# Kernel optimization log

Hardware: AMD Instinct MI355X
Metric: run time of the kernel (lower is better)

The kernel has to match this reference:

```python
import jax, jax.numpy as jnp
import numpy as np

C, H, P = 128, 4, 8  # d_model, n_heads, n_points (n_levels=1)
D = C // H


def setup_inputs() -> dict:
    key = jax.random.key(0)
    ks = jax.random.split(key, 14)
    B, Y, X = 2, 200, 200
    N = Y * X
    s = 0.05
    inp = {
        "query": jax.random.normal(ks[0], (B, N, C), jnp.float32),
        "query_pos": jax.random.normal(ks[1], (B, N, C), jnp.float32),
        # MSDeformAttn params
        "Wv": jax.random.normal(ks[2], (C, C), jnp.float32) * s,
        "bv": jnp.zeros((C,), jnp.float32),
        "Woff": jax.random.normal(ks[3], (C, H * P * 2), jnp.float32) * s,
        "boff": jax.random.normal(ks[4], (H * P * 2,), jnp.float32) * s,
        "Wattn": jax.random.normal(ks[5], (C, H * P), jnp.float32) * s,
        "battn": jnp.zeros((H * P,), jnp.float32),
        "Wout1": jax.random.normal(ks[6], (C, C), jnp.float32) * s,  # MSDeformAttn.output_proj
        "bout1": jnp.zeros((C,), jnp.float32),
        "Wout2": jax.random.normal(ks[7], (C, C), jnp.float32) * s,  # wrapper output_proj
        "bout2": jnp.zeros((C,), jnp.float32),
        "Y": Y,
        "X": X,
    }
    return inp


def _deform_attn(q, v_in, Wv, bv, Woff, boff, Wattn, battn, Wout1, bout1, Y, X):
    B, N, _ = q.shape
    # reference points: grid centers, stacked (y, x) normalized (as in source)
    ref_y = (jnp.arange(Y, dtype=jnp.float32) + 0.5) / Y
    ref_x = (jnp.arange(X, dtype=jnp.float32) + 0.5) / X
    ry, rx = jnp.meshgrid(ref_y, ref_x, indexing="ij")
    ref = jnp.stack([ry.reshape(-1), rx.reshape(-1)], -1)  # (N, 2)

    value = (v_in @ Wv + bv).reshape(B, Y, X, H, D).transpose(0, 3, 1, 2, 4)  # (B,H,Y,X,D)
    off = (q @ Woff + boff).reshape(B, N, H, P, 2)
    attn = jax.nn.softmax((q @ Wattn + battn).reshape(B, N, H, P), axis=-1)

    # offset normalizer = (W, H) = (X, Y); loc = ref + off/norm  (faithful to source)
    norm = jnp.array([X, Y], jnp.float32)
    loc = ref[None, :, None, None, :] + off / norm  # (B,N,H,P,2)

    # grid_sample bilinear, align_corners=False, zero padding; channel 0 = x, 1 = y
    gx = loc[..., 0] * X - 0.5
    gy = loc[..., 1] * Y - 0.5
    x0 = jnp.floor(gx)
    y0 = jnp.floor(gy)
    wx1 = gx - x0
    wy1 = gy - y0
    x0i = x0.astype(jnp.int32)
    y0i = y0.astype(jnp.int32)

    b_idx = jnp.arange(B)[:, None, None, None]
    h_idx = jnp.arange(H)[None, None, :, None]

    def gather(yi, xi, w):
        valid = (yi >= 0) & (yi < Y) & (xi >= 0) & (xi < X)
        yc = jnp.clip(yi, 0, Y - 1)
        xc = jnp.clip(xi, 0, X - 1)
        v = value[b_idx, h_idx, yc, xc]  # (B,N,H,P,D)
        return v * (w * valid)[..., None]

    sampled = (
        gather(y0i, x0i, (1 - wy1) * (1 - wx1))
        + gather(y0i, x0i + 1, (1 - wy1) * wx1)
        + gather(y0i + 1, x0i, wy1 * (1 - wx1))
        + gather(y0i + 1, x0i + 1, wy1 * wx1)
    )
    out = (sampled * attn[..., None]).sum(axis=3).reshape(B, N, C)
    return out @ Wout1 + bout1


def reference(query, query_pos, Wv, bv, Woff, boff, Wattn, battn, Wout1, bout1, Wout2, bout2, Y, X):
    residual = query
    q = query + query_pos
    out = _deform_attn(q, q, Wv, bv, Woff, boff, Wattn, battn, Wout1, bout1, Y, X)
    out = out @ Wout2 + bout2  # wrapper output_proj; dropout in eval mode = identity
    return out + residual
```

## Files before the change

### kernel.cpp

```cpp
#include <hip/hip_runtime.h>
#include <hip/hip_bf16.h>

#define BQ 2
#define YY 200
#define XX 200
#define NQ 40000
#define CC 128
#define MTOT 80000
#define NCOL 224
#define NTILES 5000

typedef __attribute__((ext_vector_type(8))) short short8;
typedef __attribute__((ext_vector_type(4))) float f32x4;

static __device__ __forceinline__ unsigned short f2bf(float f) {
    union { float f; unsigned int u; } v; v.f = f;
    unsigned int r = v.u + 0x7FFF + ((v.u >> 16) & 1);
    return (unsigned short)(r >> 16);
}
static __device__ __forceinline__ unsigned short f2bf_hw(float f) {
    __hip_bfloat16 h = __float2bfloat16(f);
    unsigned short s;
    __builtin_memcpy(&s, &h, 2);
    return s;
}

__global__ void prep_wcat(const float* __restrict__ Wv, const float* __restrict__ Woff,
                          const float* __restrict__ Wattn, unsigned short* __restrict__ WcatT) {
    int idx = blockIdx.x * 256 + threadIdx.x;
    if (idx >= NCOL * CC) return;
    int c = idx >> 7, k = idx & 127;
    float w = (c < 128) ? Wv[k * 128 + c]
            : (c < 192) ? Woff[k * 64 + (c - 128)]
                        : Wattn[k * 32 + (c - 192)];
    WcatT[c * 128 + k] = f2bf(w);
}

__global__ void prep_w12(const float* __restrict__ Wout1, const float* __restrict__ Wout2,
                         const float* __restrict__ bout1, const float* __restrict__ bout2,
                         unsigned short* __restrict__ W12T, float* __restrict__ b12) {
    int idx = blockIdx.x * 256 + threadIdx.x;
    int c = idx >> 7, k = idx & 127;
    float s = 0.f;
    for (int j = 0; j < 128; ++j) s += Wout1[k * 128 + j] * Wout2[j * 128 + c];
    W12T[c * 128 + k] = f2bf(s);
    if (k == 0) {
        float t = bout2[c];
        for (int j = 0; j < 128; ++j) t += bout1[j] * Wout2[j * 128 + c];
        b12[c] = t;
    }
}

__global__ __launch_bounds__(256) void g1_kernel(
    const float* __restrict__ query, const float* __restrict__ qpos,
    const unsigned short* __restrict__ WcatT,
    const float* __restrict__ bv, const float* __restrict__ boff, const float* __restrict__ battn,
    unsigned short* __restrict__ value_bf, float* __restrict__ off_out, float* __restrict__ logits_out)
{
    const int tid = threadIdx.x;
    const int lane = tid & 63;
    const int arow = lane & 15, kq = lane >> 4;
    const int wid = blockIdx.x * 4 + (tid >> 6);
    const int nw = gridDim.x * 4;

    float bias[14];
#pragma unroll
    for (int t = 0; t < 8; ++t) bias[t] = bv[t * 16 + arow];
#pragma unroll
    for (int t = 0; t < 4; ++t) bias[8 + t] = boff[t * 16 + arow];
#pragma unroll
    for (int t = 0; t < 2; ++t) bias[12 + t] = battn[t * 16 + arow];

    const char* Bb = (const char*)WcatT + (arow * 256 + kq * 16);

    for (int tile = wid; tile < NTILES; tile += nw) {
        const float4* pq = (const float4*)(query + (size_t)(tile * 16 + arow) * 128 + kq * 8);
        const float4* pp = (const float4*)(qpos  + (size_t)(tile * 16 + arow) * 128 + kq * 8);

        float4 xa[8], xb[8];
#pragma unroll
        for (int ks = 0; ks < 4; ++ks) {
            xa[2 * ks]     = pq[8 * ks];
            xa[2 * ks + 1] = pq[8 * ks + 1];
            xb[2 * ks]     = pp[8 * ks];
            xb[2 * ks + 1] = pp[8 * ks + 1];
        }

        short8 af[4];
#pragma unroll
        for (int ks = 0; ks < 4; ++ks) {
            const float* u = (const float*)&xa[2 * ks];
            const float* v = (const float*)&xb[2 * ks];
            short8 a;
#pragma unroll
            for (int j = 0; j < 8; ++j) a[j] = (short)f2bf_hw(u[j] + v[j]);
            af[ks] = a;
        }

        f32x4 acc[14];
#pragma unroll
        for (int t = 0; t < 14; ++t) acc[t] = (f32x4){0.f, 0.f, 0.f, 0.f};

#pragma unroll
        for (int ks = 0; ks < 4; ++ks) {
#pragma unroll
            for (int t = 0; t < 14; ++t) {
                short8 b = *(const short8*)(Bb + t * 4096 + ks * 64);
                acc[t] = __builtin_amdgcn_mfma_f32_16x16x32_bf16(af[ks], b, acc[t], 0, 0, 0);
            }
        }

#pragma unroll
        for (int t = 0; t < 14; ++t) {
#pragma unroll
            for (int rr = 0; rr < 4; ++rr) {
                size_t grow = (size_t)(tile * 16 + kq * 4 + rr);
                float vv = acc[t][rr] + bias[t];
                if (t < 8)
                    value_bf[grow * 128 + t * 16 + arow] = f2bf_hw(vv);
                else if (t < 12)
                    off_out[grow * 64 + (t - 8) * 16 + arow] = vv;
                else
                    logits_out[grow * 32 + (t - 12) * 16 + arow] = vv;
            }
        }
    }
}

__global__ __launch_bounds__(256) void sample_kernel(
    const unsigned short* __restrict__ value_bf, const float* __restrict__ off_in,
    const float* __restrict__ logits, unsigned short* __restrict__ sampled)
{
    __shared__ int S[8][32][8];

    const int tid = threadIdx.x;
    const int qi = tid >> 5;
    const int lane = tid & 31;
    const int r = blockIdx.x * 8 + qi;
    const int b = (r >= NQ) ? 1 : 0;
    const int n = r - b * NQ;
    const int yq = n / XX, xq = n - yq * XX;

    {
        float lg = logits[(size_t)r * 32 + lane];
        float m = lg;
        m = fmaxf(m, __shfl_xor(m, 1));
        m = fmaxf(m, __shfl_xor(m, 2));
        m = fmaxf(m, __shfl_xor(m, 4));
        float e = __expf(lg - m);
        float s = e;
        s += __shfl_xor(s, 1);
        s += __shfl_xor(s, 2);
        s += __shfl_xor(s, 4);
        float aw = e / s;

        float2 o = ((const float2*)(off_in + (size_t)r * 64))[lane];
        float gx = (float)yq + o.x;
        float gy = (float)xq + o.y;
        float fx = floorf(gx), fy = floorf(gy);
        int x0 = (int)fx, y0 = (int)fy;
        float wx1 = gx - fx, wy1 = gy - fy;
        float vx0 = ((unsigned)x0 < XX) ? 1.f : 0.f;
        float vx1 = ((unsigned)(x0 + 1) < XX) ? 1.f : 0.f;
        float vy0 = ((unsigned)y0 < YY) ? 1.f : 0.f;
        float vy1 = ((unsigned)(y0 + 1) < YY) ? 1.f : 0.f;
        int x0c = min(max(x0, 0), XX - 1);
        int x1c = min(max(x0 + 1, 0), XX - 1);
        int y0c = min(max(y0, 0), YY - 1);
        int y1c = min(max(y0 + 1, 0), YY - 1);
        int hb = (lane >> 3) * 64;
        int rowA = y0c * XX, rowB = y1c * XX;
        int4 addrs;
        addrs.x = (rowA + x0c) * 256 + hb;
        addrs.y = (rowA + x1c) * 256 + hb;
        addrs.z = (rowB + x0c) * 256 + hb;
        addrs.w = (rowB + x1c) * 256 + hb;
        int4 wts;
        wts.x = __float_as_int((1.f - wx1) * vx0);
        wts.y = __float_as_int(wx1 * vx1);
        wts.z = __float_as_int(aw * (1.f - wy1) * vy0);
        wts.w = __float_as_int(aw * wy1 * vy1);
        *(int4*)&S[qi][lane][0] = addrs;
        *(int4*)&S[qi][lane][4] = wts;
    }
    __syncthreads();

    const char* vb = (const char*)(value_bf + (size_t)b * NQ * 128);
    const int cb = (lane & 15) * 4;
    const int g16 = lane >> 4;

    float2 acc[2];
    acc[0] = make_float2(0.f, 0.f);
    acc[1] = make_float2(0.f, 0.f);

#pragma unroll
    for (int i = 0; i < 16; ++i) {
        const int hp = g16 * 16 + i;
        int4 ai = *(const int4*)&S[qi][hp][0];
        int4 wi = *(const int4*)&S[qi][hp][4];
        float wxa = __int_as_float(wi.x);
        float wxb = __int_as_float(wi.y);
        float wya = __int_as_float(wi.z);
        float wyb = __int_as_float(wi.w);

        unsigned int u00 = *(const unsigned int*)(vb + ai.x + cb);
        unsigned int u01 = *(const unsigned int*)(vb + ai.y + cb);
        unsigned int u10 = *(const unsigned int*)(vb + ai.z + cb);
        unsigned int u11 = *(const unsigned int*)(vb + ai.w + cb);

        float f00l = __uint_as_float(u00 << 16), f00h = __uint_as_float(u00 & 0xFFFF0000u);
        float f01l = __uint_as_float(u01 << 16), f01h = __uint_as_float(u01 & 0xFFFF0000u);
        float f10l = __uint_as_float(u10 << 16), f10h = __uint_as_float(u10 & 0xFFFF0000u);
        float f11l = __uint_as_float(u11 << 16), f11h = __uint_as_float(u11 & 0xFFFF0000u);

        float tal = fmaf(wxa, f00l, wxb * f01l);
        float tbl = fmaf(wxa, f10l, wxb * f11l);
        float tah = fmaf(wxa, f00h, wxb * f01h);
        float tbh = fmaf(wxa, f10h, wxb * f11h);

        const int j = i >> 3;
        acc[j].x = fmaf(wya, tal, acc[j].x);
        acc[j].x = fmaf(wyb, tbl, acc[j].x);
        acc[j].y = fmaf(wya, tah, acc[j].y);
        acc[j].y = fmaf(wyb, tbh, acc[j].y);
    }

    char* sp = (char*)(sampled + (size_t)r * 128);
#pragma unroll
    for (int j = 0; j < 2; ++j) {
        unsigned int packed = ((unsigned int)f2bf(acc[j].y) << 16) | (unsigned int)f2bf(acc[j].x);
        *(unsigned int*)(sp + (g16 * 2 + j) * 64 + cb) = packed;
    }
}

__global__ __launch_bounds__(256) void g2_kernel(
    const unsigned short* __restrict__ sampled, const unsigned short* __restrict__ W12T,
    const float* __restrict__ b12, const float* __restrict__ query, float* __restrict__ out)
{
    const int tid = threadIdx.x;
    const int lane = tid & 63;
    const int arow = lane & 15, kq = lane >> 4;
    const int wid = blockIdx.x * 4 + (tid >> 6);
    const int nw = gridDim.x * 4;

    float bias[8];
#pragma unroll
    for (int t = 0; t < 8; ++t) bias[t] = b12[t * 16 + arow];

    const char* Bb = (const char*)W12T + (arow * 256 + kq * 16);

    for (int tile = wid; tile < NTILES; tile += nw) {
        const char* pa = (const char*)sampled + (size_t)(tile * 16 + arow) * 256 + kq * 16;

        short8 af[4];
#pragma unroll
        for (int ks = 0; ks < 4; ++ks) af[ks] = *(const short8*)(pa + ks * 64);

        f32x4 acc[8];
#pragma unroll
        for (int t = 0; t < 8; ++t) acc[t] = (f32x4){0.f, 0.f, 0.f, 0.f};

#pragma unroll
        for (int ks = 0; ks < 4; ++ks) {
#pragma unroll
            for (int t = 0; t < 8; ++t) {
                short8 b = *(const short8*)(Bb + t * 4096 + ks * 64);
                acc[t] = __builtin_amdgcn_mfma_f32_16x16x32_bf16(af[ks], b, acc[t], 0, 0, 0);
            }
        }

#pragma unroll
        for (int t = 0; t < 8; ++t) {
#pragma unroll
            for (int rr = 0; rr < 4; ++rr) {
                size_t grow = (size_t)(tile * 16 + kq * 4 + rr);
                size_t idx = grow * 128 + t * 16 + arow;
                out[idx] = acc[t][rr] + bias[t] + query[idx];
            }
        }
    }
}

extern "C" void kernel_launch(void* const* d_in, const int* in_sizes, int n_in,
                              void* d_out, int out_size, void* d_ws, size_t ws_size,
                              hipStream_t stream) {
    const float* query = (const float*)d_in[0];
    const float* qpos  = (const float*)d_in[1];
    const float* Wv    = (const float*)d_in[2];
    const float* bv    = (const float*)d_in[3];
    const float* Woff  = (const float*)d_in[4];
    const float* boff  = (const float*)d_in[5];
    const float* Wattn = (const float*)d_in[6];
    const float* battn = (const float*)d_in[7];
    const float* Wout1 = (const float*)d_in[8];
    const float* bout1 = (const float*)d_in[9];
    const float* Wout2 = (const float*)d_in[10];
    const float* bout2 = (const float*)d_in[11];
    float* out = (float*)d_out;

    char* ws = (char*)d_ws;
    unsigned short* value_bf = (unsigned short*)(ws);
    float*          off_buf  = (float*)(ws + 20480000);
    float*          logits   = (float*)(ws + 40960000);
    unsigned short* sampled  = (unsigned short*)(ws + 51200000);
    unsigned short* WcatT    = (unsigned short*)(ws + 71680000);
    unsigned short* W12T     = (unsigned short*)(ws + 71680000 + 57344);
    float*          b12      = (float*)(ws + 71680000 + 57344 + 32768);

    prep_wcat<<<112, 256, 0, stream>>>(Wv, Woff, Wattn, WcatT);
    prep_w12<<<64, 256, 0, stream>>>(Wout1, Wout2, bout1, bout2, W12T, b12);
    g1_kernel<<<625, 256, 0, stream>>>(query, qpos, WcatT, bv, boff, battn,
                                       value_bf, off_buf, logits);
    sample_kernel<<<MTOT / 8, 256, 0, stream>>>(value_bf, off_buf, logits, sampled);
    g2_kernel<<<625, 256, 0, stream>>>(sampled, W12T, b12, query, out);
}
```

Baseline: 127.6 us.

## Split GEMMs by output column groups, keep weights in registers, vectorize stores

Adds a separate qsum kernel that forms query+query_pos in bf16 up front, so g1 reads bf16 activations instead of two fp32 tensors. g1 and g2 now give each block one group of output column tiles and hold that group's weight fragments in registers for the whole launch, instead of reloading weights for every tile. The MFMA operands are swapped so each lane holds contiguous outputs, which allows vectorized float4/short4 stores. The costs are an extra launch plus a round trip of the bf16 sum through memory (it reuses the sampled buffer), and each activation tile is now read by several column-group blocks.

```diff
diff --git a/kernel.cpp b/kernel.cpp
--- a/kernel.cpp
+++ b/kernel.cpp
@@ -11,6 +11,7 @@
 #define NTILES 5000
 
 typedef __attribute__((ext_vector_type(8))) short short8;
+typedef __attribute__((ext_vector_type(4))) short short4v;
 typedef __attribute__((ext_vector_type(4))) float f32x4;
 
 static __device__ __forceinline__ unsigned short f2bf(float f) {
@@ -51,77 +52,99 @@
     }
 }
 
-__global__ __launch_bounds__(256) void g1_kernel(
-    const float* __restrict__ query, const float* __restrict__ qpos,
-    const unsigned short* __restrict__ WcatT,
+__global__ __launch_bounds__(256) void qsum_kernel(const float* __restrict__ query,
+                                                   const float* __restrict__ qpos,
+                                                   unsigned short* __restrict__ qbf) {
+    const size_t total = (size_t)MTOT * CC / 8;
+    for (size_t c = (size_t)blockIdx.x * 256 + threadIdx.x; c < total;
+         c += (size_t)gridDim.x * 256) {
+        const float4* a = (const float4*)(query + c * 8);
+        const float4* b = (const float4*)(qpos + c * 8);
+        float4 a0 = a[0], a1 = a[1], b0 = b[0], b1 = b[1];
+        short8 w;
+        w[0] = (short)f2bf_hw(a0.x + b0.x); w[1] = (short)f2bf_hw(a0.y + b0.y);
+        w[2] = (short)f2bf_hw(a0.z + b0.z); w[3] = (short)f2bf_hw(a0.w + b0.w);
+        w[4] = (short)f2bf_hw(a1.x + b1.x); w[5] = (short)f2bf_hw(a1.y + b1.y);
+        w[6] = (short)f2bf_hw(a1.z + b1.z); w[7] = (short)f2bf_hw(a1.w + b1.w);
+        *(short8*)(qbf + c * 8) = w;
+    }
+}
+
+__global__ __launch_bounds__(256, 2) void g1_kernel(
+    const unsigned short* __restrict__ qbf, const unsigned short* __restrict__ WcatT,
     const float* __restrict__ bv, const float* __restrict__ boff, const float* __restrict__ battn,
     unsigned short* __restrict__ value_bf, float* __restrict__ off_out, float* __restrict__ logits_out)
 {
     const int tid = threadIdx.x;
+    const int group = blockIdx.x & 3;
+    const int gblk = blockIdx.x >> 2;
     const int lane = tid & 63;
     const int arow = lane & 15, kq = lane >> 4;
-    const int wid = blockIdx.x * 4 + (tid >> 6);
-    const int nw = gridDim.x * 4;
-
-    float bias[14];
-#pragma unroll
-    for (int t = 0; t < 8; ++t) bias[t] = bv[t * 16 + arow];
-#pragma unroll
-    for (int t = 0; t < 4; ++t) bias[8 + t] = boff[t * 16 + arow];
-#pragma unroll
-    for (int t = 0; t < 2; ++t) bias[12 + t] = battn[t * 16 + arow];
-
-    const char* Bb = (const char*)WcatT + (arow * 256 + kq * 16);
-
-    for (int tile = wid; tile < NTILES; tile += nw) {
-        const float4* pq = (const float4*)(query + (size_t)(tile * 16 + arow) * 128 + kq * 8);
-        const float4* pp = (const float4*)(qpos  + (size_t)(tile * 16 + arow) * 128 + kq * 8);
-
-        float4 xa[8], xb[8];
+    const int wid = gblk * 4 + (tid >> 6);
+    const int tg0 = group * 4;
+    const int NT = (group == 3) ? 2 : 4;
+
+    short8 bf[4][4];
+#pragma unroll
+    for (int t = 0; t < 4; ++t) {
+        if (t < NT) {
+#pragma unroll
+            for (int ks = 0; ks < 4; ++ks)
+                bf[t][ks] = *(const short8*)(WcatT + (size_t)((tg0 + t) * 16 + arow) * 128 + ks * 32 + kq * 8);
+        }
+    }
+
+    f32x4 biasv[4];
+#pragma unroll
+    for (int t = 0; t < 4; ++t) {
+        if (t < NT) {
+            const float* bp = (group < 2) ? (bv + (tg0 + t) * 16 + kq * 4)
+                            : (group == 2) ? (boff + (tg0 + t - 8) * 16 + kq * 4)
+                                           : (battn + (tg0 + t - 12) * 16 + kq * 4);
+            float4 b4 = *(const float4*)bp;
+            biasv[t] = (f32x4){b4.x, b4.y, b4.z, b4.w};
+        }
+    }
+
+    for (int tile = wid; tile < NTILES; tile += 1024) {
+        const char* pa = (const char*)qbf + (size_t)(tile * 16 + arow) * 256 + kq * 16;
+        short8 af[4];
+#pragma unroll
+        for (int ks = 0; ks < 4; ++ks) af[ks] = *(const short8*)(pa + ks * 64);
+
+        f32x4 acc[4];
+#pragma unroll
+        for (int t = 0; t < 4; ++t) acc[t] = biasv[t];
+
 #pragma unroll
         for (int ks = 0; ks < 4; ++ks) {
-            xa[2 * ks]     = pq[8 * ks];
-            xa[2 * ks + 1] = pq[8 * ks + 1];
-            xb[2 * ks]     = pp[8 * ks];
-            xb[2 * ks + 1] = pp[8 * ks + 1];
-        }
-
-        short8 af[4];
-#pragma unroll
-        for (int ks = 0; ks < 4; ++ks) {
-            const float* u = (const float*)&xa[2 * ks];
-            const float* v = (const float*)&xb[2 * ks];
-            short8 a;
-#pragma unroll
-            for (int j = 0; j < 8; ++j) a[j] = (short)f2bf_hw(u[j] + v[j]);
-            af[ks] = a;
-        }
-
-        f32x4 acc[14];
-#pragma unroll
-        for (int t = 0; t < 14; ++t) acc[t] = (f32x4){0.f, 0.f, 0.f, 0.f};
-
-#pragma unroll
-        for (int ks = 0; ks < 4; ++ks) {
-#pragma unroll
-            for (int t = 0; t < 14; ++t) {
-                short8 b = *(const short8*)(Bb + t * 4096 + ks * 64);
-                acc[t] = __builtin_amdgcn_mfma_f32_16x16x32_bf16(af[ks], b, acc[t], 0, 0, 0);
+#pragma unroll
+            for (int t = 0; t < 4; ++t) {
+                if (t < NT)
+                    acc[t] = __builtin_amdgcn_mfma_f32_16x16x32_bf16(bf[t][ks], af[ks], acc[t], 0, 0, 0);
             }
         }
 
-#pragma unroll
-        for (int t = 0; t < 14; ++t) {
-#pragma unroll
-            for (int rr = 0; rr < 4; ++rr) {
-                size_t grow = (size_t)(tile * 16 + kq * 4 + rr);
-                float vv = acc[t][rr] + bias[t];
-                if (t < 8)
-                    value_bf[grow * 128 + t * 16 + arow] = f2bf_hw(vv);
-                else if (t < 12)
-                    off_out[grow * 64 + (t - 8) * 16 + arow] = vv;
-                else
-                    logits_out[grow * 32 + (t - 12) * 16 + arow] = vv;
+        const int row = tile * 16 + arow;
+        if (group < 2) {
+#pragma unroll
+            for (int t = 0; t < 4; ++t) {
+                short4v pv;
+                pv[0] = (short)f2bf_hw(acc[t][0]); pv[1] = (short)f2bf_hw(acc[t][1]);
+                pv[2] = (short)f2bf_hw(acc[t][2]); pv[3] = (short)f2bf_hw(acc[t][3]);
+                *(short4v*)(value_bf + (size_t)row * 128 + (tg0 + t) * 16 + kq * 4) = pv;
+            }
+        } else if (group == 2) {
+#pragma unroll
+            for (int t = 0; t < 4; ++t) {
+                float4 o = make_float4(acc[t][0], acc[t][1], acc[t][2], acc[t][3]);
+                *(float4*)(off_out + (size_t)row * 64 + (tg0 + t - 8) * 16 + kq * 4) = o;
+            }
+        } else {
+#pragma unroll
+            for (int t = 0; t < 2; ++t) {
+                float4 o = make_float4(acc[t][0], acc[t][1], acc[t][2], acc[t][3]);
+                *(float4*)(logits_out + (size_t)row * 32 + (tg0 + t - 12) * 16 + kq * 4) = o;
             }
         }
     }
@@ -233,50 +256,56 @@
     }
 }
 
-__global__ __launch_bounds__(256) void g2_kernel(
+__global__ __launch_bounds__(256, 2) void g2_kernel(
     const unsigned short* __restrict__ sampled, const unsigned short* __restrict__ W12T,
     const float* __restrict__ b12, const float* __restrict__ query, float* __restrict__ out)
 {
     const int tid = threadIdx.x;
+    const int group = blockIdx.x & 1;
+    const int gblk = blockIdx.x >> 1;
     const int lane = tid & 63;
     const int arow = lane & 15, kq = lane >> 4;
-    const int wid = blockIdx.x * 4 + (tid >> 6);
-    const int nw = gridDim.x * 4;
-
-    float bias[8];
-#pragma unroll
-    for (int t = 0; t < 8; ++t) bias[t] = b12[t * 16 + arow];
-
-    const char* Bb = (const char*)W12T + (arow * 256 + kq * 16);
-
-    for (int tile = wid; tile < NTILES; tile += nw) {
+    const int wid = gblk * 4 + (tid >> 6);
+    const int tg0 = group * 4;
+
+    short8 bf[4][4];
+#pragma unroll
+    for (int t = 0; t < 4; ++t)
+#pragma unroll
+        for (int ks = 0; ks < 4; ++ks)
+            bf[t][ks] = *(const short8*)(W12T + (size_t)((tg0 + t) * 16 + arow) * 128 + ks * 32 + kq * 8);
+
+    f32x4 biasv[4];
+#pragma unroll
+    for (int t = 0; t < 4; ++t) {
+        float4 b4 = *(const float4*)(b12 + (tg0 + t) * 16 + kq * 4);
+        biasv[t] = (f32x4){b4.x, b4.y, b4.z, b4.w};
+    }
+
+    for (int tile = wid; tile < NTILES; tile += 2048) {
         const char* pa = (const char*)sampled + (size_t)(tile * 16 + arow) * 256 + kq * 16;
-
         short8 af[4];
 #pragma unroll
         for (int ks = 0; ks < 4; ++ks) af[ks] = *(const short8*)(pa + ks * 64);
 
-        f32x4 acc[8];
-#pragma unroll
-        for (int t = 0; t < 8; ++t) acc[t] = (f32x4){0.f, 0.f, 0.f, 0.f};
-
-#pragma unroll
-        for (int ks = 0; ks < 4; ++ks) {
-#pragma unroll
-            for (int t = 0; t < 8; ++t) {
-                short8 b = *(const short8*)(Bb + t * 4096 + ks * 64);
-                acc[t] = __builtin_amdgcn_mfma_f32_16x16x32_bf16(af[ks], b, acc[t], 0, 0, 0);
-            }
-        }
-
-#pragma unroll
-        for (int t = 0; t < 8; ++t) {
-#pragma unroll
-            for (int rr = 0; rr < 4; ++rr) {
-                size_t grow = (size_t)(tile * 16 + kq * 4 + rr);
-                size_t idx = grow * 128 + t * 16 + arow;
-                out[idx] = acc[t][rr] + bias[t] + query[idx];
-            }
+        f32x4 acc[4];
+#pragma unroll
+        for (int t = 0; t < 4; ++t) acc[t] = biasv[t];
+
+#pragma unroll
+        for (int ks = 0; ks < 4; ++ks)
+#pragma unroll
+            for (int t = 0; t < 4; ++t)
+                acc[t] = __builtin_amdgcn_mfma_f32_16x16x32_bf16(bf[t][ks], af[ks], acc[t], 0, 0, 0);
+
+        const int row = tile * 16 + arow;
+#pragma unroll
+        for (int t = 0; t < 4; ++t) {
+            size_t idx = (size_t)row * 128 + (tg0 + t) * 16 + kq * 4;
+            float4 q4 = *(const float4*)(query + idx);
+            float4 o = make_float4(acc[t][0] + q4.x, acc[t][1] + q4.y,
+                                   acc[t][2] + q4.z, acc[t][3] + q4.w);
+            *(float4*)(out + idx) = o;
         }
     }
 }
@@ -307,10 +336,13 @@
     unsigned short* W12T     = (unsigned short*)(ws + 71680000 + 57344);
     float*          b12      = (float*)(ws + 71680000 + 57344 + 32768);
 
+    unsigned short* qbf = sampled;
+
     prep_wcat<<<112, 256, 0, stream>>>(Wv, Woff, Wattn, WcatT);
     prep_w12<<<64, 256, 0, stream>>>(Wout1, Wout2, bout1, bout2, W12T, b12);
-    g1_kernel<<<625, 256, 0, stream>>>(query, qpos, WcatT, bv, boff, battn,
-                                       value_bf, off_buf, logits);
+    qsum_kernel<<<2048, 256, 0, stream>>>(query, qpos, qbf);
+    g1_kernel<<<1024, 256, 0, stream>>>(qbf, WcatT, bv, boff, battn,
+                                        value_bf, off_buf, logits);
     sample_kernel<<<MTOT / 8, 256, 0, stream>>>(value_bf, off_buf, logits, sampled);
-    g2_kernel<<<625, 256, 0, stream>>>(sampled, W12T, b12, query, out);
-}
+    g2_kernel<<<1024, 256, 0, stream>>>(sampled, W12T, b12, query, out);
+}
```

Measured after the change: 126.2 us. No clear change (-1.1%).
